# Performance work log

Hardware: AMD Instinct MI355X
Metric: run time of the kernel (lower is better)

Reference implementation:

```python
import jax, jax.numpy as jnp
import numpy as np

H = 8          # SD1.4 heads
TAU = 0.1      # HarmCfg.tau
GAMMA = 1.0    # HarmCfg.gamma
EPS = 1e-12    # F.normalize eps


def setup_inputs() -> dict:
    key = jax.random.key(0)
    ks = jax.random.split(key, 8)
    B, S, C, K, D = 16, 4096, 320, 77, 768
    return {
        "hidden_states": jax.random.normal(ks[0], (B, S, C), jnp.float32),
        "encoder_hidden_states": jax.random.normal(ks[1], (B, K, D), jnp.float32),
        "harm_vec": jax.random.normal(ks[2], (D,), jnp.float32),
        "Wq": jax.random.normal(ks[3], (C, C), jnp.float32) * 0.02,
        "Wk": jax.random.normal(ks[4], (D, C), jnp.float32) * 0.02,
        "Wv": jax.random.normal(ks[5], (D, C), jnp.float32) * 0.02,
        "Wo": jax.random.normal(ks[6], (C, C), jnp.float32) * 0.02,
        "bo": jnp.zeros((C,), jnp.float32),
    }


def reference(hidden_states, encoder_hidden_states, harm_vec, Wq, Wk, Wv, Wo, bo):
    B, S, C = hidden_states.shape
    K = encoder_hidden_states.shape[1]
    dh = C // H
    scale = 1.0 / jnp.sqrt(jnp.asarray(dh, hidden_states.dtype))

    # projections (no bias on q/k/v, as in diffusers SD1.4)
    q = (hidden_states @ Wq).reshape(B, S, H, dh)
    k = (encoder_hidden_states @ Wk).reshape(B, K, H, dh)
    v = (encoder_hidden_states @ Wv).reshape(B, K, H, dh)

    # scores: QK^T / sqrt(dh)  -> [B, H, S, K]
    scores = jnp.einsum('bqhd,bkhd->bhqk', q, k) * scale

    # cosine-similarity harmful-token penalty (broadcast over heads and queries)
    harm = harm_vec / jnp.maximum(jnp.linalg.norm(harm_vec), EPS)
    ctx_norm = encoder_hidden_states / jnp.maximum(
        jnp.linalg.norm(encoder_hidden_states, axis=-1, keepdims=True), EPS)
    cos = jnp.einsum('bkd,d->bk', ctx_norm, harm)            # [B, K]
    penalty = jnp.maximum(cos - TAU, 0.0)                     # clamp(min=0)
    scores = scores - GAMMA * penalty[:, None, None, :]

    probs = jax.nn.softmax(scores, axis=-1)                   # dropout p=0 (eval)
    out = jnp.einsum('bhqk,bkhd->bqhd', probs, v).reshape(B, S, C)
    return out @ Wo + bo
```

## Files before the change

### kernel.cpp

```cpp
#include <hip/hip_runtime.h>
#include <hip/hip_bf16.h>

#define B_ 16
#define S_ 4096
#define C_ 320
#define KK_ 77
#define D_ 768
#define H_ 8
#define DH_ 40
#define KP_ 80
#define NP_ (H_ * KP_)
#define TAU_ 0.1f
#define GAMMA_ 1.0f
#define EPS_ 1e-12f

typedef __bf16 bf16x8 __attribute__((ext_vector_type(8)));
typedef float f32x4 __attribute__((ext_vector_type(4)));
typedef unsigned short ushort8v __attribute__((ext_vector_type(8)));
typedef unsigned int u32;

#define WAITV(N)  asm volatile("s_waitcnt vmcnt(" #N ")" ::: "memory")
#define WAITVL(N) asm volatile("s_waitcnt vmcnt(" #N ") lgkmcnt(0)" ::: "memory")
#define WAITLG()  asm volatile("s_waitcnt lgkmcnt(0)" ::: "memory")
#define BAR()     __builtin_amdgcn_s_barrier()

__device__ __forceinline__ unsigned short f2bf(float f) {
    union { float f; unsigned u; } v; v.f = f;
    unsigned r = v.u + 0x7fffu + ((v.u >> 16) & 1u);
    return (unsigned short)(r >> 16);
}

__device__ __forceinline__ void gld16(const unsigned short* g, char* l) {
    __builtin_amdgcn_global_load_lds(
        (const __attribute__((address_space(1))) u32*)g,
        (__attribute__((address_space(3))) u32*)l, 16, 0, 0);
}

__global__ __launch_bounds__(256) void build_M(const float* __restrict__ Wq,
        const float* __restrict__ Wk, const float* __restrict__ Wv,
        const float* __restrict__ Wo, unsigned short* __restrict__ Bmat) {
    const int Dk = blockIdx.x * 256 + threadIdx.x;
    const int h = blockIdx.y;
    const int which = blockIdx.z >> 2;
    const int c0 = (blockIdx.z & 3) * 80;
    __shared__ float wlds[80 * 44];
    for (int i = threadIdx.x; i < 80 * DH_; i += 256) {
        int c = i / DH_, d = i % DH_;
        wlds[c * 44 + d] = which
            ? Wo[(size_t)(h * DH_ + d) * C_ + (c0 + c)]
            : Wq[(size_t)(c0 + c) * C_ + h * DH_ + d];
    }
    float a[DH_];
    const float* Arow = (which ? Wv : Wk) + (size_t)Dk * C_ + h * DH_;
    #pragma unroll
    for (int d = 0; d < DH_; ++d) a[d] = Arow[d];
    __syncthreads();
    const float scale = 0.15811388300841898f;
    for (int c = 0; c < 80; ++c) {
        float s = 0.f;
        #pragma unroll
        for (int q = 0; q < 10; ++q) {
            float4 wv4 = *(const float4*)&wlds[c * 44 + q * 4];
            s += a[q * 4 + 0] * wv4.x + a[q * 4 + 1] * wv4.y
               + a[q * 4 + 2] * wv4.z + a[q * 4 + 3] * wv4.w;
        }
        if (!which) s *= scale;
        int n = which * 2560 + h * C_ + c0 + c;
        Bmat[(size_t)n * D_ + Dk] = f2bf(s);
    }
}

__global__ __launch_bounds__(256) void prep_ehs(const float* __restrict__ ehs,
        const float* __restrict__ harm, unsigned short* __restrict__ ehs_bf,
        float* __restrict__ pen) {
    const int w = threadIdx.x >> 6, l = threadIdx.x & 63;
    const int kk = blockIdx.x * 4 + w, b = blockIdx.y;
    const size_t obase = ((size_t)b * KP_ + kk) * D_;
    if (kk >= KK_) {
        #pragma unroll
        for (int j = 0; j < 12; ++j) ehs_bf[obase + l + j * 64] = 0;
        if (l == 0) pen[b * KP_ + kk] = 0.f;
        return;
    }
    const float* er = ehs + ((size_t)b * KK_ + kk) * D_;
    float ss = 0.f, dd = 0.f, hh = 0.f;
    #pragma unroll
    for (int j = 0; j < 12; ++j) {
        float e = er[l + j * 64], hv = harm[l + j * 64];
        ehs_bf[obase + l + j * 64] = f2bf(e);
        ss += e * e; dd += e * hv; hh += hv * hv;
    }
    #pragma unroll
    for (int off = 32; off; off >>= 1) {
        ss += __shfl_xor(ss, off);
        dd += __shfl_xor(dd, off);
        hh += __shfl_xor(hh, off);
    }
    if (l == 0) {
        float cs = dd / (fmaxf(sqrtf(ss), EPS_) * fmaxf(sqrtf(hh), EPS_));
        pen[b * KP_ + kk] = GAMMA_ * fmaxf(cs - TAU_, 0.f);
    }
}

__global__ __launch_bounds__(1024) void gemm_WpU(
        const unsigned short* __restrict__ ehs_bf,
        const unsigned short* __restrict__ Bmat,
        unsigned short* __restrict__ Wp, unsigned short* __restrict__ U) {
    const int id = blockIdx.x;
    const int b = id & 15, nt = id >> 4;
    const int tid = threadIdx.x, w = tid >> 6, l = tid & 63;
    const int lrow = l & 15, lgrp = l >> 4, lk = lgrp * 8;
    __shared__ unsigned short Al[80 * 768];
    char* lds = (char*)Al;

    const unsigned short* Ag = ehs_bf + (size_t)b * KP_ * D_;
    #pragma unroll
    for (int it = 0; it < 8; ++it) {
        int ch = tid + it * 1024;
        if (ch < 7680) {
            int byte = ch * 16, row = byte / 1536;
            int a = byte ^ ((row & 7) << 4);
            *(ushort8v*)(lds + a) = *(const ushort8v*)(Ag + ch * 8);
        }
    }
    const int n0 = nt * 512 + w * 32;
    const unsigned short* Br = Bmat + (size_t)(n0 + lrow) * D_ + lk;
    bf16x8 bC[2], bN[2];
    #pragma unroll
    for (int nf = 0; nf < 2; ++nf)
        bC[nf] = *(const bf16x8*)(Br + (size_t)nf * 16 * D_);
    __syncthreads();

    f32x4 acc[5][2];
    #pragma unroll
    for (int mf = 0; mf < 5; ++mf)
        #pragma unroll
        for (int nf = 0; nf < 2; ++nf) acc[mf][nf] = (f32x4){0.f, 0.f, 0.f, 0.f};
    #pragma unroll
    for (int ks = 0; ks < D_ / 32; ++ks) {
        if (ks < D_ / 32 - 1) {
            #pragma unroll
            for (int nf = 0; nf < 2; ++nf)
                bN[nf] = *(const bf16x8*)(Br + (size_t)nf * 16 * D_ + (ks + 1) * 32);
        }
        bf16x8 af[5];
        #pragma unroll
        for (int mf = 0; mf < 5; ++mf) {
            int row = mf * 16 + lrow;
            int a = (row * 1536 + (ks * 32 + lk) * 2) ^ ((row & 7) << 4);
            af[mf] = *(const bf16x8*)(lds + a);
        }
        __builtin_amdgcn_s_setprio(1);
        #pragma unroll
        for (int mf = 0; mf < 5; ++mf)
            #pragma unroll
            for (int nf = 0; nf < 2; ++nf)
                acc[mf][nf] = __builtin_amdgcn_mfma_f32_16x16x32_bf16(
                    af[mf], bC[nf], acc[mf][nf], 0, 0, 0);
        __builtin_amdgcn_s_setprio(0);
        #pragma unroll
        for (int nf = 0; nf < 2; ++nf) bC[nf] = bN[nf];
    }
    #pragma unroll
    for (int nf = 0; nf < 2; ++nf) {
        const int col = n0 + nf * 16 + lrow;
        if (col < 2560) {
            const int h = col / C_, c = col % C_;
            #pragma unroll
            for (int mf = 0; mf < 5; ++mf)
                #pragma unroll
                for (int r = 0; r < 4; ++r) {
                    int kk = mf * 16 + lgrp * 4 + r;
                    Wp[((size_t)b * NP_ + h * KP_ + kk) * C_ + c] = f2bf(acc[mf][nf][r]);
                }
        } else {
            const int n2 = col - 2560;
            const int h = n2 / C_, c = n2 % C_;
            #pragma unroll
            for (int mf = 0; mf < 5; ++mf)
                #pragma unroll
                for (int r = 0; r < 4; ++r) {
                    int kk = mf * 16 + lgrp * 4 + r;
                    U[((size_t)b * C_ + c) * NP_ + h * KP_ + kk] = f2bf(acc[mf][nf][r]);
                }
        }
    }
}

__global__ __launch_bounds__(512, 2) void fused_attn(
        const float* __restrict__ hs, const unsigned short* __restrict__ Wp,
        const unsigned short* __restrict__ U, const float* __restrict__ pen,
        const float* __restrict__ bo, float* __restrict__ out) {
    const int id = blockIdx.x;
    const int xcd = id & 7, rest = id >> 3;
    const int b = xcd * 2 + (rest >> 6);
    const int s0 = (rest & 63) * 64;
    __shared__ __align__(16) char smem[163840];
    char* HS = smem;
    char* WB = smem + 40960;
    char* PB = smem;
    char* U0 = smem + 81920;
    char* U1 = smem + 122880;
    const int tid = threadIdx.x, w = tid >> 6, l = tid & 63;
    const int lrow = l & 15, lgrp = l >> 4, lk = lgrp * 8;
    const int h = w;
    const int mgrp = w & 1, ngrp = w >> 1;

    const unsigned short* Wpb = Wp + ((size_t)b * NP_) * C_;
    const unsigned short* Ub  = U  + ((size_t)b * C_) * NP_;

    auto stage_wp = [&](int s) {
        #pragma unroll
        for (int j = 0; j < 10; ++j) {
            int ch = w * 640 + j * 64 + l;
            int n = ch >> 3, q = ch & 7;
            gld16(Wpb + (size_t)n * C_ + s * 64 + ((q ^ (n & 7)) << 3),
                  WB + ch * 16);
        }
    };
    auto stage_u = [&](int t, char* buf) {
        #pragma unroll
        for (int j = 0; j < 5; ++j) {
            int ch = w * 320 + j * 64 + l;
            int c = ch >> 3, q = ch & 7;
            gld16(Ub + (size_t)c * NP_ + t * 64 + ((q ^ (c & 7)) << 3),
                  buf + ch * 16);
        }
    };

    float4 pv4[5];
    #pragma unroll
    for (int nf = 0; nf < 5; ++nf)
        pv4[nf] = *(const float4*)(pen + b * KP_ + nf * 16 + lgrp * 4);
    const float4* hv = (const float4*)(hs + ((size_t)b * S_ + s0) * C_);
    #pragma unroll
    for (int it = 0; it < 10; ++it) {
        int i = tid + it * 512;
        float4 v = hv[i];
        int r = i / 80, c = (i * 4) % C_;
        ushort4 u;
        u.x = f2bf(v.x); u.y = f2bf(v.y); u.z = f2bf(v.z); u.w = f2bf(v.w);
        int a = (r * 640 + c * 2) ^ ((r & 7) << 4);
        *(ushort4*)(HS + a) = u;
    }
    __syncthreads();
    stage_wp(0);

    f32x4 acc[5][4];
    #pragma unroll
    for (int nf = 0; nf < 5; ++nf)
        #pragma unroll
        for (int mf = 0; mf < 4; ++mf) acc[nf][mf] = (f32x4){0.f, 0.f, 0.f, 0.f};
    #pragma unroll
    for (int s = 0; s < 5; ++s) {
        WAITV(0);
        BAR();
        bf16x8 bC[5][2], hf[4][2];
        #pragma unroll
        for (int nf = 0; nf < 5; ++nf) {
            int n = h * KP_ + nf * 16 + lrow;
            #pragma unroll
            for (int ss = 0; ss < 2; ++ss)
                bC[nf][ss] = *(const bf16x8*)(WB + n * 128 +
                    ((ss * 64 + lgrp * 16) ^ ((n & 7) << 4)));
        }
        #pragma unroll
        for (int mf = 0; mf < 4; ++mf) {
            int row = mf * 16 + lrow;
            #pragma unroll
            for (int ss = 0; ss < 2; ++ss) {
                int ks32 = 2 * s + ss;
                int a = (row * 640 + (ks32 * 32 + lk) * 2) ^ ((row & 7) << 4);
                hf[mf][ss] = *(const bf16x8*)(HS + a);
            }
        }
        WAITLG();
        BAR();
        if (s < 4) stage_wp(s + 1);
        __builtin_amdgcn_s_setprio(1);
        #pragma unroll
        for (int ss = 0; ss < 2; ++ss)
            #pragma unroll
            for (int nf = 0; nf < 5; ++nf)
                #pragma unroll
                for (int mf = 0; mf < 4; ++mf)
                    acc[nf][mf] = __builtin_amdgcn_mfma_f32_16x16x32_bf16(
                        bC[nf][ss], hf[mf][ss], acc[nf][mf], 0, 0, 0);
        __builtin_amdgcn_s_setprio(0);
    }

    stage_u(0, U0);
    stage_u(1, U1);

    float inv4[4];
    #pragma unroll
    for (int mf = 0; mf < 4; ++mf) {
        float mx = -1e30f;
        #pragma unroll
        for (int nf = 0; nf < 5; ++nf)
            #pragma unroll
            for (int r = 0; r < 4; ++r) {
                float x = acc[nf][mf][r] - ((const float*)&pv4[nf])[r];
                if (nf == 4 && r >= 1) x = (lgrp == 3) ? -1e30f : x;
                acc[nf][mf][r] = x;
                mx = fmaxf(mx, x);
            }
        mx = fmaxf(mx, __shfl_xor(mx, 16));
        mx = fmaxf(mx, __shfl_xor(mx, 32));
        float s = 0.f;
        #pragma unroll
        for (int nf = 0; nf < 5; ++nf)
            #pragma unroll
            for (int r = 0; r < 4; ++r) {
                float e = __expf(acc[nf][mf][r] - mx);
                acc[nf][mf][r] = e; s += e;
            }
        s += __shfl_xor(s, 16);
        s += __shfl_xor(s, 32);
        inv4[mf] = 1.f / s;
    }

    #pragma unroll
    for (int mf = 0; mf < 4; ++mf) {
        const int m = mf * 16 + lrow;
        const float inv = inv4[mf];
        #pragma unroll
        for (int nf = 0; nf < 5; ++nf) {
            ushort4 u;
            u.x = f2bf(acc[nf][mf][0] * inv);
            u.y = f2bf(acc[nf][mf][1] * inv);
            u.z = f2bf(acc[nf][mf][2] * inv);
            u.w = f2bf(acc[nf][mf][3] * inv);
            int a = (m * 1280 + (h * KP_ + nf * 16 + lgrp * 4) * 2) ^ ((m & 7) << 4);
            *(ushort4*)(PB + a) = u;
        }
    }
    WAITVL(5);
    BAR();

    f32x4 acc2[5][2];
    #pragma unroll
    for (int nf = 0; nf < 5; ++nf)
        #pragma unroll
        for (int mf = 0; mf < 2; ++mf) acc2[nf][mf] = (f32x4){0.f, 0.f, 0.f, 0.f};
    #pragma unroll
    for (int t = 0; t < 10; ++t) {
        if (t > 0) {
            if (t < 9) { WAITV(5); } else { WAITV(0); }
            BAR();
        }
        char* ub = (t & 1) ? U1 : U0;
        bf16x8 pa[2][2], uf[5][2];
        #pragma unroll
        for (int mf = 0; mf < 2; ++mf) {
            int m = mgrp * 32 + mf * 16 + lrow;
            #pragma unroll
            for (int ss = 0; ss < 2; ++ss) {
                int a = (m * 1280 + (t * 128 + ss * 64 + lgrp * 16)) ^ ((m & 7) << 4);
                pa[mf][ss] = *(const bf16x8*)(PB + a);
            }
        }
        #pragma unroll
        for (int nf = 0; nf < 5; ++nf) {
            int c = ngrp * KP_ + nf * 16 + lrow;
            #pragma unroll
            for (int ss = 0; ss < 2; ++ss)
                uf[nf][ss] = *(const bf16x8*)(ub + c * 128 +
                    ((ss * 64 + lgrp * 16) ^ ((c & 7) << 4)));
        }
        WAITLG();
        BAR();
        if (t < 8) stage_u(t + 2, ub);
        __builtin_amdgcn_s_setprio(1);
        #pragma unroll
        for (int ss = 0; ss < 2; ++ss)
            #pragma unroll
            for (int nf = 0; nf < 5; ++nf)
                #pragma unroll
                for (int mf = 0; mf < 2; ++mf)
                    acc2[nf][mf] = __builtin_amdgcn_mfma_f32_16x16x32_bf16(
                        pa[mf][ss], uf[nf][ss], acc2[nf][mf], 0, 0, 0);
        __builtin_amdgcn_s_setprio(0);
    }

    float bov[5];
    #pragma unroll
    for (int nf = 0; nf < 5; ++nf) bov[nf] = bo[ngrp * KP_ + nf * 16 + lrow];
    float* op = out + ((size_t)b * S_ + s0) * C_;
    #pragma unroll
    for (int mf = 0; mf < 2; ++mf)
        #pragma unroll
        for (int r = 0; r < 4; ++r)
            #pragma unroll
            for (int nf = 0; nf < 5; ++nf)
                op[(size_t)(mgrp * 32 + mf * 16 + lgrp * 4 + r) * C_ +
                   ngrp * KP_ + nf * 16 + lrow] = acc2[nf][mf][r] + bov[nf];
}

extern "C" void kernel_launch(void* const* d_in, const int* in_sizes, int n_in,
                              void* d_out, int out_size, void* d_ws, size_t ws_size,
                              hipStream_t stream) {
    const float* hs   = (const float*)d_in[0];
    const float* ehs  = (const float*)d_in[1];
    const float* harm = (const float*)d_in[2];
    const float* Wq   = (const float*)d_in[3];
    const float* Wk   = (const float*)d_in[4];
    const float* Wv   = (const float*)d_in[5];
    const float* Wo   = (const float*)d_in[6];
    const float* bo   = (const float*)d_in[7];
    float* out = (float*)d_out;

    char* ws = (char*)d_ws;
    unsigned short* ehs_bf = (unsigned short*)(ws);
    unsigned short* Bmat   = (unsigned short*)(ws + 1966080);
    float*          pen    = (float*)        (ws + 9830400);
    unsigned short* Wp     = (unsigned short*)(ws + 9835520);
    unsigned short* U      = (unsigned short*)(ws + 16389120);

    build_M <<<dim3(3, 8, 8),  256, 0, stream>>>(Wq, Wk, Wv, Wo, Bmat);
    prep_ehs<<<dim3(20, 16),   256, 0, stream>>>(ehs, harm, ehs_bf, pen);
    gemm_WpU<<<dim3(160),     1024, 0, stream>>>(ehs_bf, Bmat, Wp, U);
    fused_attn<<<dim3(1024),   512, 0, stream>>>(hs, Wp, U, pen, bo, out);
}
```

Baseline: 161.4 us.

## Double query tile per block to reuse staged Wp and U weights

Each block now processes 128 query rows instead of 64, so each per-batch Wp and U chunk loaded into shared memory feeds twice as many MFMAs, and the grid is halved. Because the full probability tile no longer fits in LDS, it is split in two halves by head: four waves write their probabilities, the first half of the U contraction runs, then the other four waves write theirs. This doubles the accumulator registers per wave (two score tiles plus a larger output tile), which risks register pressure or spills at the declared launch bounds and leaves fewer blocks to spread across CUs.

Measured after the change: 179.9 us. 1.11x slower.

```diff
diff --git a/kernel.cpp b/kernel.cpp
--- a/kernel.cpp
+++ b/kernel.cpp
@@ -193,18 +193,18 @@
         const float* __restrict__ bo, float* __restrict__ out) {
     const int id = blockIdx.x;
     const int xcd = id & 7, rest = id >> 3;
-    const int b = xcd * 2 + (rest >> 6);
-    const int s0 = (rest & 63) * 64;
+    const int b = xcd * 2 + (rest >> 5);
+    const int s0 = (rest & 31) * 128;
     __shared__ __align__(16) char smem[163840];
     char* HS = smem;
-    char* WB = smem + 40960;
+    char* WB = smem + 81920;
     char* PB = smem;
     char* U0 = smem + 81920;
     char* U1 = smem + 122880;
     const int tid = threadIdx.x, w = tid >> 6, l = tid & 63;
     const int lrow = l & 15, lgrp = l >> 4, lk = lgrp * 8;
     const int h = w;
-    const int mgrp = w & 1, ngrp = w >> 1;
+    const int mhat = w & 1, chat = w >> 1;
 
     const unsigned short* Wpb = Wp + ((size_t)b * NP_) * C_;
     const unsigned short* Ub  = U  + ((size_t)b * C_) * NP_;
@@ -218,23 +218,19 @@
                   WB + ch * 16);
         }
     };
-    auto stage_u = [&](int t, char* buf) {
+    auto stage_u = [&](int nt, char* buf) {
         #pragma unroll
         for (int j = 0; j < 5; ++j) {
             int ch = w * 320 + j * 64 + l;
             int c = ch >> 3, q = ch & 7;
-            gld16(Ub + (size_t)c * NP_ + t * 64 + ((q ^ (c & 7)) << 3),
+            gld16(Ub + (size_t)c * NP_ + nt * 64 + ((q ^ (c & 7)) << 3),
                   buf + ch * 16);
         }
     };
 
-    float4 pv4[5];
-    #pragma unroll
-    for (int nf = 0; nf < 5; ++nf)
-        pv4[nf] = *(const float4*)(pen + b * KP_ + nf * 16 + lgrp * 4);
     const float4* hv = (const float4*)(hs + ((size_t)b * S_ + s0) * C_);
     #pragma unroll
-    for (int it = 0; it < 10; ++it) {
+    for (int it = 0; it < 20; ++it) {
         int i = tid + it * 512;
         float4 v = hv[i];
         int r = i / 80, c = (i * 4) % C_;
@@ -246,155 +242,194 @@
     __syncthreads();
     stage_wp(0);
 
-    f32x4 acc[5][4];
+    f32x4 accA[5][4], accB[5][4];
     #pragma unroll
     for (int nf = 0; nf < 5; ++nf)
         #pragma unroll
-        for (int mf = 0; mf < 4; ++mf) acc[nf][mf] = (f32x4){0.f, 0.f, 0.f, 0.f};
+        for (int mf = 0; mf < 4; ++mf) {
+            accA[nf][mf] = (f32x4){0.f, 0.f, 0.f, 0.f};
+            accB[nf][mf] = (f32x4){0.f, 0.f, 0.f, 0.f};
+        }
     #pragma unroll
     for (int s = 0; s < 5; ++s) {
         WAITV(0);
         BAR();
-        bf16x8 bC[5][2], hf[4][2];
-        #pragma unroll
-        for (int nf = 0; nf < 5; ++nf) {
-            int n = h * KP_ + nf * 16 + lrow;
-            #pragma unroll
-            for (int ss = 0; ss < 2; ++ss)
-                bC[nf][ss] = *(const bf16x8*)(WB + n * 128 +
+        #pragma unroll
+        for (int ss = 0; ss < 2; ++ss) {
+            bf16x8 bC[5], hfA[4], hfB[4];
+            #pragma unroll
+            for (int nf = 0; nf < 5; ++nf) {
+                int n = h * KP_ + nf * 16 + lrow;
+                bC[nf] = *(const bf16x8*)(WB + n * 128 +
                     ((ss * 64 + lgrp * 16) ^ ((n & 7) << 4)));
-        }
+            }
+            #pragma unroll
+            for (int mf = 0; mf < 4; ++mf) {
+                int ks32 = 2 * s + ss;
+                int rowA = mf * 16 + lrow;
+                hfA[mf] = *(const bf16x8*)(HS +
+                    ((rowA * 640 + (ks32 * 32 + lk) * 2) ^ ((rowA & 7) << 4)));
+                int rowB = 64 + mf * 16 + lrow;
+                hfB[mf] = *(const bf16x8*)(HS +
+                    ((rowB * 640 + (ks32 * 32 + lk) * 2) ^ ((rowB & 7) << 4)));
+            }
+            WAITLG();
+            if (ss == 1) {
+                BAR();
+                if (s < 4) stage_wp(s + 1);
+            }
+            __builtin_amdgcn_s_setprio(1);
+            #pragma unroll
+            for (int nf = 0; nf < 5; ++nf)
+                #pragma unroll
+                for (int mf = 0; mf < 4; ++mf) {
+                    accA[nf][mf] = __builtin_amdgcn_mfma_f32_16x16x32_bf16(
+                        bC[nf], hfA[mf], accA[nf][mf], 0, 0, 0);
+                    accB[nf][mf] = __builtin_amdgcn_mfma_f32_16x16x32_bf16(
+                        bC[nf], hfB[mf], accB[nf][mf], 0, 0, 0);
+                }
+            __builtin_amdgcn_s_setprio(0);
+        }
+    }
+
+    float4 pv4[5];
+    #pragma unroll
+    for (int nf = 0; nf < 5; ++nf)
+        pv4[nf] = *(const float4*)(pen + b * KP_ + nf * 16 + lgrp * 4);
+    WAITV(0);
+
+    ushort4 pk[2][4][5];
+    #pragma unroll
+    for (int X = 0; X < 2; ++X) {
         #pragma unroll
         for (int mf = 0; mf < 4; ++mf) {
-            int row = mf * 16 + lrow;
+            f32x4* acc = X ? &accB[0][mf] : &accA[0][mf];
+            float mx = -1e30f;
+            #pragma unroll
+            for (int nf = 0; nf < 5; ++nf)
+                #pragma unroll
+                for (int r = 0; r < 4; ++r) {
+                    float x = (X ? accB[nf][mf][r] : accA[nf][mf][r])
+                              - ((const float*)&pv4[nf])[r];
+                    if (nf == 4 && r >= 1) x = (lgrp == 3) ? -1e30f : x;
+                    if (X) accB[nf][mf][r] = x; else accA[nf][mf][r] = x;
+                    mx = fmaxf(mx, x);
+                }
+            mx = fmaxf(mx, __shfl_xor(mx, 16));
+            mx = fmaxf(mx, __shfl_xor(mx, 32));
+            float sum = 0.f;
+            #pragma unroll
+            for (int nf = 0; nf < 5; ++nf)
+                #pragma unroll
+                for (int r = 0; r < 4; ++r) {
+                    float e = __expf((X ? accB[nf][mf][r] : accA[nf][mf][r]) - mx);
+                    if (X) accB[nf][mf][r] = e; else accA[nf][mf][r] = e;
+                    sum += e;
+                }
+            sum += __shfl_xor(sum, 16);
+            sum += __shfl_xor(sum, 32);
+            float inv = 1.f / sum;
+            #pragma unroll
+            for (int nf = 0; nf < 5; ++nf) {
+                ushort4 u;
+                u.x = f2bf((X ? accB[nf][mf][0] : accA[nf][mf][0]) * inv);
+                u.y = f2bf((X ? accB[nf][mf][1] : accA[nf][mf][1]) * inv);
+                u.z = f2bf((X ? accB[nf][mf][2] : accA[nf][mf][2]) * inv);
+                u.w = f2bf((X ? accB[nf][mf][3] : accA[nf][mf][3]) * inv);
+                pk[X][mf][nf] = u;
+            }
+        }
+    }
+
+    if (h < 4) {
+        #pragma unroll
+        for (int X = 0; X < 2; ++X)
+            #pragma unroll
+            for (int mf = 0; mf < 4; ++mf) {
+                int row = X * 64 + mf * 16 + lrow;
+                #pragma unroll
+                for (int nf = 0; nf < 5; ++nf) {
+                    int col = (h & 3) * KP_ + nf * 16 + lgrp * 4;
+                    *(ushort4*)(PB + ((row * 640 + col * 2) ^ ((row & 7) << 4)))
+                        = pk[X][mf][nf];
+                }
+            }
+    }
+
+    f32x4 acc2[5][4];
+    #pragma unroll
+    for (int nf = 0; nf < 5; ++nf)
+        #pragma unroll
+        for (int mf = 0; mf < 4; ++mf) acc2[nf][mf] = (f32x4){0.f, 0.f, 0.f, 0.f};
+    #pragma unroll
+    for (int p = 0; p < 2; ++p) {
+        stage_u(p * 5 + 0, U0);
+        stage_u(p * 5 + 1, U1);
+        WAITVL(5);
+        BAR();
+        #pragma unroll
+        for (int t = 0; t < 5; ++t) {
+            char* ub = (t & 1) ? U1 : U0;
             #pragma unroll
             for (int ss = 0; ss < 2; ++ss) {
-                int ks32 = 2 * s + ss;
-                int a = (row * 640 + (ks32 * 32 + lk) * 2) ^ ((row & 7) << 4);
-                hf[mf][ss] = *(const bf16x8*)(HS + a);
-            }
-        }
-        WAITLG();
-        BAR();
-        if (s < 4) stage_wp(s + 1);
-        __builtin_amdgcn_s_setprio(1);
-        #pragma unroll
-        for (int ss = 0; ss < 2; ++ss)
+                bf16x8 pa[4], uf[5];
+                #pragma unroll
+                for (int mf = 0; mf < 4; ++mf) {
+                    int row = mhat * 64 + mf * 16 + lrow;
+                    pa[mf] = *(const bf16x8*)(PB + ((row * 640 +
+                        t * 128 + ss * 64 + lgrp * 16) ^ ((row & 7) << 4)));
+                }
+                #pragma unroll
+                for (int nf = 0; nf < 5; ++nf) {
+                    int c = chat * KP_ + nf * 16 + lrow;
+                    uf[nf] = *(const bf16x8*)(ub + c * 128 +
+                        ((ss * 64 + lgrp * 16) ^ ((c & 7) << 4)));
+                }
+                WAITLG();
+                if (ss == 1) {
+                    BAR();
+                    if (t < 3) stage_u(p * 5 + t + 2, ub);
+                }
+                __builtin_amdgcn_s_setprio(1);
+                #pragma unroll
+                for (int nf = 0; nf < 5; ++nf)
+                    #pragma unroll
+                    for (int mf = 0; mf < 4; ++mf)
+                        acc2[nf][mf] = __builtin_amdgcn_mfma_f32_16x16x32_bf16(
+                            pa[mf], uf[nf], acc2[nf][mf], 0, 0, 0);
+                __builtin_amdgcn_s_setprio(0);
+            }
+            if (t < 3)      { WAITV(5); BAR(); }
+            else if (t == 3){ WAITV(0); BAR(); }
+        }
+        if (p == 0 && h >= 4) {
+            #pragma unroll
+            for (int X = 0; X < 2; ++X)
+                #pragma unroll
+                for (int mf = 0; mf < 4; ++mf) {
+                    int row = X * 64 + mf * 16 + lrow;
+                    #pragma unroll
+                    for (int nf = 0; nf < 5; ++nf) {
+                        int col = (h & 3) * KP_ + nf * 16 + lgrp * 4;
+                        *(ushort4*)(PB + ((row * 640 + col * 2) ^ ((row & 7) << 4)))
+                            = pk[X][mf][nf];
+                    }
+                }
+        }
+    }
+
+    float bov[5];
+    #pragma unroll
+    for (int nf = 0; nf < 5; ++nf) bov[nf] = bo[chat * KP_ + nf * 16 + lrow];
+    float* op = out + ((size_t)b * S_ + s0 + mhat * 64) * C_;
+    #pragma unroll
+    for (int mf = 0; mf < 4; ++mf)
+        #pragma unroll
+        for (int r = 0; r < 4; ++r)
             #pragma unroll
             for (int nf = 0; nf < 5; ++nf)
-                #pragma unroll
-                for (int mf = 0; mf < 4; ++mf)
-                    acc[nf][mf] = __builtin_amdgcn_mfma_f32_16x16x32_bf16(
-                        bC[nf][ss], hf[mf][ss], acc[nf][mf], 0, 0, 0);
-        __builtin_amdgcn_s_setprio(0);
-    }
-
-    stage_u(0, U0);
-    stage_u(1, U1);
-
-    float inv4[4];
-    #pragma unroll
-    for (int mf = 0; mf < 4; ++mf) {
-        float mx = -1e30f;
-        #pragma unroll
-        for (int nf = 0; nf < 5; ++nf)
-            #pragma unroll
-            for (int r = 0; r < 4; ++r) {
-                float x = acc[nf][mf][r] - ((const float*)&pv4[nf])[r];
-                if (nf == 4 && r >= 1) x = (lgrp == 3) ? -1e30f : x;
-                acc[nf][mf][r] = x;
-                mx = fmaxf(mx, x);
-            }
-        mx = fmaxf(mx, __shfl_xor(mx, 16));
-        mx = fmaxf(mx, __shfl_xor(mx, 32));
-        float s = 0.f;
-        #pragma unroll
-        for (int nf = 0; nf < 5; ++nf)
-            #pragma unroll
-            for (int r = 0; r < 4; ++r) {
-                float e = __expf(acc[nf][mf][r] - mx);
-                acc[nf][mf][r] = e; s += e;
-            }
-        s += __shfl_xor(s, 16);
-        s += __shfl_xor(s, 32);
-        inv4[mf] = 1.f / s;
-    }
-
-    #pragma unroll
-    for (int mf = 0; mf < 4; ++mf) {
-        const int m = mf * 16 + lrow;
-        const float inv = inv4[mf];
-        #pragma unroll
-        for (int nf = 0; nf < 5; ++nf) {
-            ushort4 u;
-            u.x = f2bf(acc[nf][mf][0] * inv);
-            u.y = f2bf(acc[nf][mf][1] * inv);
-            u.z = f2bf(acc[nf][mf][2] * inv);
-            u.w = f2bf(acc[nf][mf][3] * inv);
-            int a = (m * 1280 + (h * KP_ + nf * 16 + lgrp * 4) * 2) ^ ((m & 7) << 4);
-            *(ushort4*)(PB + a) = u;
-        }
-    }
-    WAITVL(5);
-    BAR();
-
-    f32x4 acc2[5][2];
-    #pragma unroll
-    for (int nf = 0; nf < 5; ++nf)
-        #pragma unroll
-        for (int mf = 0; mf < 2; ++mf) acc2[nf][mf] = (f32x4){0.f, 0.f, 0.f, 0.f};
-    #pragma unroll
-    for (int t = 0; t < 10; ++t) {
-        if (t > 0) {
-            if (t < 9) { WAITV(5); } else { WAITV(0); }
-            BAR();
-        }
-        char* ub = (t & 1) ? U1 : U0;
-        bf16x8 pa[2][2], uf[5][2];
-        #pragma unroll
-        for (int mf = 0; mf < 2; ++mf) {
-            int m = mgrp * 32 + mf * 16 + lrow;
-            #pragma unroll
-            for (int ss = 0; ss < 2; ++ss) {
-                int a = (m * 1280 + (t * 128 + ss * 64 + lgrp * 16)) ^ ((m & 7) << 4);
-                pa[mf][ss] = *(const bf16x8*)(PB + a);
-            }
-        }
-        #pragma unroll
-        for (int nf = 0; nf < 5; ++nf) {
-            int c = ngrp * KP_ + nf * 16 + lrow;
-            #pragma unroll
-            for (int ss = 0; ss < 2; ++ss)
-                uf[nf][ss] = *(const bf16x8*)(ub + c * 128 +
-                    ((ss * 64 + lgrp * 16) ^ ((c & 7) << 4)));
-        }
-        WAITLG();
-        BAR();
-        if (t < 8) stage_u(t + 2, ub);
-        __builtin_amdgcn_s_setprio(1);
-        #pragma unroll
-        for (int ss = 0; ss < 2; ++ss)
-            #pragma unroll
-            for (int nf = 0; nf < 5; ++nf)
-                #pragma unroll
-                for (int mf = 0; mf < 2; ++mf)
-                    acc2[nf][mf] = __builtin_amdgcn_mfma_f32_16x16x32_bf16(
-                        pa[mf][ss], uf[nf][ss], acc2[nf][mf], 0, 0, 0);
-        __builtin_amdgcn_s_setprio(0);
-    }
-
-    float bov[5];
-    #pragma unroll
-    for (int nf = 0; nf < 5; ++nf) bov[nf] = bo[ngrp * KP_ + nf * 16 + lrow];
-    float* op = out + ((size_t)b * S_ + s0) * C_;
-    #pragma unroll
-    for (int mf = 0; mf < 2; ++mf)
-        #pragma unroll
-        for (int r = 0; r < 4; ++r)
-            #pragma unroll
-            for (int nf = 0; nf < 5; ++nf)
-                op[(size_t)(mgrp * 32 + mf * 16 + lgrp * 4 + r) * C_ +
-                   ngrp * KP_ + nf * 16 + lrow] = acc2[nf][mf][r] + bov[nf];
+                op[(size_t)(mf * 16 + lgrp * 4 + r) * C_ +
+                   chat * KP_ + nf * 16 + lrow] = acc2[nf][mf][r] + bov[nf];
 }
 
 extern "C" void kernel_launch(void* const* d_in, const int* in_sizes, int n_in,
@@ -420,5 +455,5 @@
     build_M <<<dim3(3, 8, 8),  256, 0, stream>>>(Wq, Wk, Wv, Wo, Bmat);
     prep_ehs<<<dim3(20, 16),   256, 0, stream>>>(ehs, harm, ehs_bf, pen);
     gemm_WpU<<<dim3(160),     1024, 0, stream>>>(ehs_bf, Bmat, Wp, U);
-    fused_attn<<<dim3(1024),   512, 0, stream>>>(hs, Wp, U, pen, bo, out);
-}
+    fused_attn<<<dim3(512),    512, 0, stream>>>(hs, Wp, U, pen, bo, out);
+}
```

## Halve LDS footprint to fit more blocks per CU in fused attention

Applied to the files above, without the earlier changes.

Shared memory drops from 160KB to 80KB, and launch bounds change from 2 to 4 blocks of 512 threads. To fit, the Wp stage now streams 32-wide K slices over 10 steps instead of 64-wide over 5. The full P matrix is no longer written to LDS: each wave keeps its probabilities in registers and writes them into small double-buffered P chunks just before each PV step. U staging becomes single-buffered with a full wait and barrier every iteration. More resident waves are meant to hide latency, at the cost of extra barriers, less prefetch depth and tighter register limits that may cause spills.

Result: slower. 333.4 us (+106.6%).

```diff
diff --git a/kernel.cpp b/kernel.cpp
--- a/kernel.cpp
+++ b/kernel.cpp
@@ -20,7 +20,6 @@
 typedef unsigned int u32;
 
 #define WAITV(N)  asm volatile("s_waitcnt vmcnt(" #N ")" ::: "memory")
-#define WAITVL(N) asm volatile("s_waitcnt vmcnt(" #N ") lgkmcnt(0)" ::: "memory")
 #define WAITLG()  asm volatile("s_waitcnt lgkmcnt(0)" ::: "memory")
 #define BAR()     __builtin_amdgcn_s_barrier()
 
@@ -187,7 +186,7 @@
     }
 }
 
-__global__ __launch_bounds__(512, 2) void fused_attn(
+__global__ __launch_bounds__(512, 4) void fused_attn(
         const float* __restrict__ hs, const unsigned short* __restrict__ Wp,
         const unsigned short* __restrict__ U, const float* __restrict__ pen,
         const float* __restrict__ bo, float* __restrict__ out) {
@@ -195,43 +194,39 @@
     const int xcd = id & 7, rest = id >> 3;
     const int b = xcd * 2 + (rest >> 6);
     const int s0 = (rest & 63) * 64;
-    __shared__ __align__(16) char smem[163840];
-    char* HS = smem;
-    char* WB = smem + 40960;
-    char* PB = smem;
-    char* U0 = smem + 81920;
-    char* U1 = smem + 122880;
+    __shared__ __align__(16) char smem[81920];
+    char* HS  = smem;
+    char* WB  = smem + 40960;
+    char* PC0 = smem;
+    char* PC1 = smem + 8192;
+    char* UB  = smem + 16384;
     const int tid = threadIdx.x, w = tid >> 6, l = tid & 63;
-    const int lrow = l & 15, lgrp = l >> 4, lk = lgrp * 8;
-    const int h = w;
-    const int mgrp = w & 1, ngrp = w >> 1;
-
-    const unsigned short* Wpb = Wp + ((size_t)b * NP_) * C_;
-    const unsigned short* Ub  = U  + ((size_t)b * C_) * NP_;
+    const int lrow = l & 15, lgrp = l >> 4;
+    const int mgrp = w & 1, cgrp = w >> 1;
+
+    const unsigned short* Wpb = Wp + (size_t)b * NP_ * C_;
+    const unsigned short* Ub  = U  + (size_t)b * C_ * NP_;
 
     auto stage_wp = [&](int s) {
         #pragma unroll
-        for (int j = 0; j < 10; ++j) {
-            int ch = w * 640 + j * 64 + l;
-            int n = ch >> 3, q = ch & 7;
-            gld16(Wpb + (size_t)n * C_ + s * 64 + ((q ^ (n & 7)) << 3),
-                  WB + ch * 16);
+        for (int j = 0; j < 5; ++j) {
+            int ch = w * 320 + j * 64 + l;
+            int r = ch >> 3, d = ch & 7;
+            int q = d ^ (r & 7);
+            int n = (q < 4) ? r : r + 320;
+            gld16(Wpb + (size_t)n * C_ + s * 32 + (q & 3) * 8, WB + ch * 16);
         }
     };
-    auto stage_u = [&](int t, char* buf) {
+    auto stage_u = [&](int t) {
         #pragma unroll
         for (int j = 0; j < 5; ++j) {
             int ch = w * 320 + j * 64 + l;
             int c = ch >> 3, q = ch & 7;
             gld16(Ub + (size_t)c * NP_ + t * 64 + ((q ^ (c & 7)) << 3),
-                  buf + ch * 16);
+                  UB + ch * 16);
         }
     };
 
-    float4 pv4[5];
-    #pragma unroll
-    for (int nf = 0; nf < 5; ++nf)
-        pv4[nf] = *(const float4*)(pen + b * KP_ + nf * 16 + lgrp * 4);
     const float4* hv = (const float4*)(hs + ((size_t)b * S_ + s0) * C_);
     #pragma unroll
     for (int it = 0; it < 10; ++it) {
@@ -252,47 +247,42 @@
         #pragma unroll
         for (int mf = 0; mf < 4; ++mf) acc[nf][mf] = (f32x4){0.f, 0.f, 0.f, 0.f};
     #pragma unroll
-    for (int s = 0; s < 5; ++s) {
+    for (int s = 0; s < 10; ++s) {
         WAITV(0);
         BAR();
-        bf16x8 bC[5][2], hf[4][2];
+        bf16x8 bC[5], hf[4];
         #pragma unroll
         for (int nf = 0; nf < 5; ++nf) {
-            int n = h * KP_ + nf * 16 + lrow;
-            #pragma unroll
-            for (int ss = 0; ss < 2; ++ss)
-                bC[nf][ss] = *(const bf16x8*)(WB + n * 128 +
-                    ((ss * 64 + lgrp * 16) ^ ((n & 7) << 4)));
+            int n = w * KP_ + nf * 16 + lrow;
+            int r = (w < 4) ? n : n - 320;
+            int dq = ((w < 4) ? lgrp : (4 | lgrp)) ^ (r & 7);
+            bC[nf] = *(const bf16x8*)(WB + r * 128 + (dq << 4));
         }
         #pragma unroll
         for (int mf = 0; mf < 4; ++mf) {
             int row = mf * 16 + lrow;
-            #pragma unroll
-            for (int ss = 0; ss < 2; ++ss) {
-                int ks32 = 2 * s + ss;
-                int a = (row * 640 + (ks32 * 32 + lk) * 2) ^ ((row & 7) << 4);
-                hf[mf][ss] = *(const bf16x8*)(HS + a);
-            }
+            hf[mf] = *(const bf16x8*)(HS +
+                ((row * 640 + s * 64 + lgrp * 16) ^ ((row & 7) << 4)));
         }
         WAITLG();
         BAR();
-        if (s < 4) stage_wp(s + 1);
+        if (s < 9) stage_wp(s + 1);
+        else       stage_u(0);
         __builtin_amdgcn_s_setprio(1);
         #pragma unroll
-        for (int ss = 0; ss < 2; ++ss)
-            #pragma unroll
-            for (int nf = 0; nf < 5; ++nf)
-                #pragma unroll
-                for (int mf = 0; mf < 4; ++mf)
-                    acc[nf][mf] = __builtin_amdgcn_mfma_f32_16x16x32_bf16(
-                        bC[nf][ss], hf[mf][ss], acc[nf][mf], 0, 0, 0);
+        for (int nf = 0; nf < 5; ++nf)
+            #pragma unroll
+            for (int mf = 0; mf < 4; ++mf)
+                acc[nf][mf] = __builtin_amdgcn_mfma_f32_16x16x32_bf16(
+                    bC[nf], hf[mf], acc[nf][mf], 0, 0, 0);
         __builtin_amdgcn_s_setprio(0);
     }
 
-    stage_u(0, U0);
-    stage_u(1, U1);
-
-    float inv4[4];
+    float4 pv4[5];
+    #pragma unroll
+    for (int nf = 0; nf < 5; ++nf)
+        pv4[nf] = *(const float4*)(pen + b * KP_ + nf * 16 + lgrp * 4);
+    ushort4 pk[4][5];
     #pragma unroll
     for (int mf = 0; mf < 4; ++mf) {
         float mx = -1e30f;
@@ -307,23 +297,17 @@
             }
         mx = fmaxf(mx, __shfl_xor(mx, 16));
         mx = fmaxf(mx, __shfl_xor(mx, 32));
-        float s = 0.f;
+        float sum = 0.f;
         #pragma unroll
         for (int nf = 0; nf < 5; ++nf)
             #pragma unroll
             for (int r = 0; r < 4; ++r) {
                 float e = __expf(acc[nf][mf][r] - mx);
-                acc[nf][mf][r] = e; s += e;
+                acc[nf][mf][r] = e; sum += e;
             }
-        s += __shfl_xor(s, 16);
-        s += __shfl_xor(s, 32);
-        inv4[mf] = 1.f / s;
-    }
-
-    #pragma unroll
-    for (int mf = 0; mf < 4; ++mf) {
-        const int m = mf * 16 + lrow;
-        const float inv = inv4[mf];
+        sum += __shfl_xor(sum, 16);
+        sum += __shfl_xor(sum, 32);
+        float inv = 1.f / sum;
         #pragma unroll
         for (int nf = 0; nf < 5; ++nf) {
             ushort4 u;
@@ -331,11 +315,23 @@
             u.y = f2bf(acc[nf][mf][1] * inv);
             u.z = f2bf(acc[nf][mf][2] * inv);
             u.w = f2bf(acc[nf][mf][3] * inv);
-            int a = (m * 1280 + (h * KP_ + nf * 16 + lgrp * 4) * 2) ^ ((m & 7) << 4);
-            *(ushort4*)(PB + a) = u;
-        }
-    }
-    WAITVL(5);
+            pk[mf][nf] = u;
+        }
+    }
+
+    if (w == 0) {
+        #pragma unroll
+        for (int nf = 0; nf < 4; ++nf) {
+            int kk2 = (nf * 16 + lgrp * 4) * 2;
+            #pragma unroll
+            for (int mf = 0; mf < 4; ++mf) {
+                int row = mf * 16 + lrow;
+                *(ushort4*)(PC0 + ((row * 128 + kk2) ^ ((row & 7) << 4))) = pk[mf][nf];
+            }
+        }
+    }
+    WAITV(0);
+    WAITLG();
     BAR();
 
     f32x4 acc2[5][2];
@@ -345,32 +341,42 @@
         for (int mf = 0; mf < 2; ++mf) acc2[nf][mf] = (f32x4){0.f, 0.f, 0.f, 0.f};
     #pragma unroll
     for (int t = 0; t < 10; ++t) {
-        if (t > 0) {
-            if (t < 9) { WAITV(5); } else { WAITV(0); }
-            BAR();
-        }
-        char* ub = (t & 1) ? U1 : U0;
+        char* pc = (t & 1) ? PC1 : PC0;
         bf16x8 pa[2][2], uf[5][2];
         #pragma unroll
         for (int mf = 0; mf < 2; ++mf) {
-            int m = mgrp * 32 + mf * 16 + lrow;
-            #pragma unroll
-            for (int ss = 0; ss < 2; ++ss) {
-                int a = (m * 1280 + (t * 128 + ss * 64 + lgrp * 16)) ^ ((m & 7) << 4);
-                pa[mf][ss] = *(const bf16x8*)(PB + a);
-            }
+            int row = mgrp * 32 + mf * 16 + lrow;
+            #pragma unroll
+            for (int ss = 0; ss < 2; ++ss)
+                pa[mf][ss] = *(const bf16x8*)(pc +
+                    ((row * 128 + ss * 64 + lgrp * 16) ^ ((row & 7) << 4)));
         }
         #pragma unroll
         for (int nf = 0; nf < 5; ++nf) {
-            int c = ngrp * KP_ + nf * 16 + lrow;
+            int c = cgrp * KP_ + nf * 16 + lrow;
             #pragma unroll
             for (int ss = 0; ss < 2; ++ss)
-                uf[nf][ss] = *(const bf16x8*)(ub + c * 128 +
+                uf[nf][ss] = *(const bf16x8*)(UB + c * 128 +
                     ((ss * 64 + lgrp * 16) ^ ((c & 7) << 4)));
         }
         WAITLG();
         BAR();
-        if (t < 8) stage_u(t + 2, ub);
+        if (t < 9) {
+            char* pcn = ((t + 1) & 1) ? PC1 : PC0;
+            #pragma unroll
+            for (int nf = 0; nf < 5; ++nf) {
+                if (((w * KP_ + nf * 16) >> 6) == t + 1) {
+                    int kk2 = (w * KP_ + nf * 16 + lgrp * 4 - (t + 1) * 64) * 2;
+                    #pragma unroll
+                    for (int mf = 0; mf < 4; ++mf) {
+                        int row = mf * 16 + lrow;
+                        *(ushort4*)(pcn + ((row * 128 + kk2) ^ ((row & 7) << 4)))
+                            = pk[mf][nf];
+                    }
+                }
+            }
+            stage_u(t + 1);
+        }
         __builtin_amdgcn_s_setprio(1);
         #pragma unroll
         for (int ss = 0; ss < 2; ++ss)
@@ -381,11 +387,16 @@
                     acc2[nf][mf] = __builtin_amdgcn_mfma_f32_16x16x32_bf16(
                         pa[mf][ss], uf[nf][ss], acc2[nf][mf], 0, 0, 0);
         __builtin_amdgcn_s_setprio(0);
+        if (t < 9) {
+            WAITV(0);
+            WAITLG();
+            BAR();
+        }
     }
 
     float bov[5];
     #pragma unroll
-    for (int nf = 0; nf < 5; ++nf) bov[nf] = bo[ngrp * KP_ + nf * 16 + lrow];
+    for (int nf = 0; nf < 5; ++nf) bov[nf] = bo[cgrp * KP_ + nf * 16 + lrow];
     float* op = out + ((size_t)b * S_ + s0) * C_;
     #pragma unroll
     for (int mf = 0; mf < 2; ++mf)
@@ -394,7 +405,7 @@
             #pragma unroll
             for (int nf = 0; nf < 5; ++nf)
                 op[(size_t)(mgrp * 32 + mf * 16 + lgrp * 4 + r) * C_ +
-                   ngrp * KP_ + nf * 16 + lrow] = acc2[nf][mf][r] + bov[nf];
+                   cgrp * KP_ + nf * 16 + lrow] = acc2[nf][mf][r] + bov[nf];
 }
 
 extern "C" void kernel_launch(void* const* d_in, const int* in_sizes, int n_in,
```
